# Optimization experiments

Hardware: AMD Instinct MI355X
Metric: run time of the kernel (lower is better)

The kernel has to match this reference:

```python
import jax, jax.numpy as jnp
import numpy as np

N_NODES = 100000
NEG_SLOPE = 0.2


def gat_conv(x, edge_index, W, a_src, a_dst, bias):
    """PyG GATConv, heads=1, concat, add_self_loops=True."""
    N = x.shape[0]
    loop = jnp.arange(N, dtype=edge_index.dtype)
    src = jnp.concatenate([edge_index[0], loop])  # message sources j
    dst = jnp.concatenate([edge_index[1], loop])  # message targets i
    h = x @ W                                      # [N, out]
    asrc = h @ a_src                               # [N]
    adst = h @ a_dst                               # [N]
    e = jax.nn.leaky_relu(asrc[src] + adst[dst], NEG_SLOPE)   # [E+N]
    m = jax.ops.segment_max(e, dst, num_segments=N)           # per-dst max
    w = jnp.exp(e - jax.lax.stop_gradient(m)[dst])
    denom = jax.ops.segment_sum(w, dst, num_segments=N)
    alpha = w / denom[dst]                                     # softmax per dst
    out = jax.ops.segment_sum(alpha[:, None] * h[src], dst, num_segments=N)
    return out + bias


def setup_inputs() -> dict:
    key = jax.random.key(0)
    ks = jax.random.split(key, 16)
    N, E, D = N_NODES, 3200000, 128
    x = jax.random.normal(ks[0], (N, D), dtype=jnp.float32)
    edge_index = jax.random.randint(ks[1], (2, E), 0, N, dtype=jnp.int64)
    def glorot(k, shape):
        fan = sum(shape)
        return jax.random.uniform(k, shape, jnp.float32, -1.0, 1.0) * np.sqrt(6.0 / fan)
    return {
        "x": x,
        "edge_index": edge_index,
        "W1": glorot(ks[2], (D, 16)),
        "a1_src": glorot(ks[3], (16,)),
        "a1_dst": glorot(ks[4], (16,)),
        "b1": jnp.zeros((16,), jnp.float32),
        "W2": glorot(ks[5], (16, 10)),
        "a2_src": glorot(ks[6], (10,)),
        "a2_dst": glorot(ks[7], (10,)),
        "b2": jnp.zeros((10,), jnp.float32),
        "Wl1": glorot(ks[8], (10, 10)),
        "bl1": jnp.zeros((10,), jnp.float32),
        "Wl2": glorot(ks[9], (10, 1)),
        "bl2": jnp.zeros((1,), jnp.float32),
    }


def reference(x, edge_index, W1, a1_src, a1_dst, b1, W2, a2_src, a2_dst, b2,
              Wl1, bl1, Wl2, bl2):
    h = gat_conv(x, edge_index, W1, a1_src, a1_dst, b1)
    h = jax.nn.relu(h)
    h = gat_conv(h, edge_index, W2, a2_src, a2_dst, b2)
    h = h @ Wl1 + bl1
    h = jax.nn.relu(h)
    return h @ Wl2 + bl2  # [N, 1]
```

## Files before the change

### kernel.cpp

```cpp
#include <hip/hip_runtime.h>
#include <hip/hip_fp16.h>


#define NEG 0.2f
#define FSH 7
#define BNODES 128
#define NSBMAX 1024
#define CAP 4608
#define TILE 8192
#define PES 9

__device__ __forceinline__ float lrelu(float x) { return x > 0.0f ? x : NEG * x; }

__device__ __forceinline__ unsigned fenc(float f) {
    unsigned u = __float_as_uint(f);
    return (u & 0x80000000u) ? ~u : (u | 0x80000000u);
}
__device__ __forceinline__ float fdec(unsigned e) {
    return (e & 0x80000000u) ? __uint_as_float(e & 0x7FFFFFFFu) : __uint_as_float(~e);
}

__device__ __forceinline__ float4 ldh4(const __half* h, size_t off) {
    uint2 u = *(const uint2*)(h + off);
    __half2 a = *(__half2*)&u.x, b = *(__half2*)&u.y;
    float2 fa = __half22float2(a), fb = __half22float2(b);
    return make_float4(fa.x, fa.y, fb.x, fb.y);
}

__global__ __launch_bounds__(256) void k_init(unsigned* g, int* chist, int NSB) {
    int i = blockIdx.x * 256 + threadIdx.x;
    if (i < NSB) chist[i] = 0;
    if (i < 2) g[i] = 0u;
}

__global__ __launch_bounds__(256) void k_gemm1(
    const float* __restrict__ x, const float* __restrict__ W1,
    const float* __restrict__ a1s, const float* __restrict__ a1d,
    __half* __restrict__ h1, float* __restrict__ s1, float* __restrict__ d1,
    unsigned* __restrict__ gmax, int N)
{
    __shared__ float sW[128 * 16];
    __shared__ float sx[64 * 132];
    __shared__ float wm[4];
    int tid = threadIdx.x;
    for (int i = tid; i < 2048; i += 256) sW[i] = W1[i];
    int node0 = blockIdx.x * 64;
    for (int i = tid; i < 64 * 32; i += 256) {
        int row = i >> 5, c4 = i & 31;
        int n = node0 + row;
        float4 v = make_float4(0.f, 0.f, 0.f, 0.f);
        if (n < N) v = ((const float4*)x)[(size_t)n * 32 + c4];
        *(float4*)&sx[row * 132 + c4 * 4] = v;
    }
    __syncthreads();

    int node = node0 + (tid >> 2);
    int grp  = tid & 3;
    const float* xr = &sx[(tid >> 2) * 132];
    float4 acc = make_float4(0.f, 0.f, 0.f, 0.f);
#pragma unroll 8
    for (int j = 0; j < 128; ++j) {
        float xv = xr[j];
        float4 w = *(const float4*)&sW[j * 16 + grp * 4];
        acc.x += xv * w.x; acc.y += xv * w.y; acc.z += xv * w.z; acc.w += xv * w.w;
    }
    float4 as = ((const float4*)a1s)[grp];
    float4 ad = ((const float4*)a1d)[grp];
    float sv = acc.x * as.x + acc.y * as.y + acc.z * as.z + acc.w * as.w;
    float dv = acc.x * ad.x + acc.y * ad.y + acc.z * ad.z + acc.w * ad.w;
    sv += __shfl_xor(sv, 1); sv += __shfl_xor(sv, 2);
    dv += __shfl_xor(dv, 1); dv += __shfl_xor(dv, 2);
    if (node < N) {
        __half2 p0 = __floats2half2_rn(acc.x, acc.y);
        __half2 p1 = __floats2half2_rn(acc.z, acc.w);
        uint2 u; u.x = *(unsigned*)&p0; u.y = *(unsigned*)&p1;
        *(uint2*)&h1[(size_t)node * 16 + grp * 4] = u;
        if (grp == 0) { s1[node] = sv; d1[node] = dv; }
    }
    float m = (node < N) ? sv : -3.4e38f;
#pragma unroll
    for (int off = 32; off >= 1; off >>= 1) m = fmaxf(m, __shfl_xor(m, off));
    if ((tid & 63) == 0) wm[tid >> 6] = m;
    __syncthreads();
    if (tid == 0) {
        float b = fmaxf(fmaxf(wm[0], wm[1]), fmaxf(wm[2], wm[3]));
        atomicMax(gmax, fenc(b));
    }
}

__global__ __launch_bounds__(256) void k_chist(const int* __restrict__ edst,
                                               int* __restrict__ chist, int E, int NSB) {
    __shared__ int lc[NSBMAX];
    int tid = threadIdx.x;
    for (int i = tid; i < NSB; i += 256) lc[i] = 0;
    __syncthreads();
    int stride = gridDim.x * 256;
    for (int e = blockIdx.x * 256 + tid; e < E; e += stride)
        atomicAdd(&lc[edst[e] >> FSH], 1);
    __syncthreads();
    for (int i = tid; i < NSB; i += 256) { int v = lc[i]; if (v) atomicAdd(&chist[i], v); }
}

__global__ __launch_bounds__(512) void k_cboffs(const int* __restrict__ chist,
                                                int* __restrict__ cboffs, int* __restrict__ ccur,
                                                int NSB, int E) {
    __shared__ int wsum[8];
    int tid = threadIdx.x;
    int i0 = 2 * tid, i1 = i0 + 1;
    int a = (i0 < NSB) ? chist[i0] : 0;
    int b = (i1 < NSB) ? chist[i1] : 0;
    int s = a + b, pfx = s;
#pragma unroll
    for (int off = 1; off < 64; off <<= 1) {
        int t = __shfl_up(pfx, off, 64);
        if ((tid & 63) >= off) pfx += t;
    }
    if ((tid & 63) == 63) wsum[tid >> 6] = pfx;
    __syncthreads();
    int carry = 0;
    for (int w = 0; w < (tid >> 6); ++w) carry += wsum[w];
    int excl = pfx + carry - s;
    if (i0 < NSB) { cboffs[i0] = excl;     ccur[i0 * 16] = excl; }
    if (i1 < NSB) { cboffs[i1] = excl + a; ccur[i1 * 16] = excl + a; }
    if (tid == 0) cboffs[NSB] = E;
}

__global__ __launch_bounds__(512) void k_csplit(
    const int* __restrict__ esrc, const int* __restrict__ edst,
    int* __restrict__ ccur, unsigned* __restrict__ pairs, int E, int NSB)
{
    __shared__ unsigned lsrt[TILE];
    __shared__ int lhist[NSBMAX];
    __shared__ int lofs[NSBMAX];
    __shared__ int gbase[NSBMAX];
    __shared__ int wsum[8];
    int tid = threadIdx.x;
    int base = blockIdx.x * TILE;
    int tcnt = min(TILE, E - base);
    for (int i = tid; i < NSB; i += 512) lhist[i] = 0;
    __syncthreads();
    for (int i = tid; i < tcnt; i += 512)
        atomicAdd(&lhist[edst[base + i] >> FSH], 1);
    __syncthreads();
    int i0 = 2 * tid, i1 = i0 + 1;
    int a = (i0 < NSB) ? lhist[i0] : 0;
    int b = (i1 < NSB) ? lhist[i1] : 0;
    int s = a + b, pfx = s;
#pragma unroll
    for (int off = 1; off < 64; off <<= 1) {
        int t = __shfl_up(pfx, off, 64);
        if ((tid & 63) >= off) pfx += t;
    }
    if ((tid & 63) == 63) wsum[tid >> 6] = pfx;
    __syncthreads();
    int carry = 0;
    for (int w = 0; w < (tid >> 6); ++w) carry += wsum[w];
    int excl = pfx + carry - s;
    if (i0 < NSB) {
        lofs[i0] = excl;
        gbase[i0] = a ? atomicAdd(&ccur[i0 * 16], a) : 0;
    }
    if (i1 < NSB) {
        lofs[i1] = excl + a;
        gbase[i1] = b ? atomicAdd(&ccur[i1 * 16], b) : 0;
    }
    __syncthreads();
    if (i0 < NSB) lhist[i0] = lofs[i0];
    if (i1 < NSB) lhist[i1] = lofs[i1];
    __syncthreads();
    for (int i = tid; i < tcnt; i += 512) {
        int e = base + i;
        int d = edst[e], srcv = esrc[e];
        int pos = atomicAdd(&lhist[d >> FSH], 1);
        lsrt[pos] = ((unsigned)(d & (BNODES - 1)) << 17) | (unsigned)srcv;
    }
    __syncthreads();
    for (int i = tid; i < tcnt; i += 512) {
        int lo = 0, hi = NSB - 1;
        while (lo < hi) { int mid = (lo + hi + 1) >> 1; if (lofs[mid] <= i) lo = mid; else hi = mid - 1; }
        pairs[gbase[lo] + (i - lofs[lo])] = lsrt[i];
    }
}

__global__ __launch_bounds__(512) void k_agg1(
    const int* __restrict__ boffs, const unsigned* __restrict__ pairs,
    const float* __restrict__ s1, const float* __restrict__ d1, const __half* __restrict__ h1,
    const float* __restrict__ b1, const float* __restrict__ W2,
    const float* __restrict__ a2s, const float* __restrict__ a2d,
    __half* __restrict__ h2, float* __restrict__ s2, float* __restrict__ d2,
    const unsigned* __restrict__ gmax1p, unsigned* __restrict__ gmax2, int N)
{
    __shared__ unsigned srt[CAP];
    __shared__ float accs[BNODES * 17];
    __shared__ int lcnt[BNODES];
    __shared__ int lofs[BNODES + 1];
    __shared__ float dds[BNODES], mbs[BNODES];
    __shared__ float sW[160], sb[16], sas[16], sad[16];
    __shared__ int wsum[8];
    __shared__ float wm[8];

    int tid = threadIdx.x;
    int fb = blockIdx.x;
    if (tid < 160) sW[tid] = W2[tid];
    if (tid < 16) {
        sb[tid]  = b1[tid];
        sas[tid] = (tid < 10) ? a2s[tid] : 0.f;
        sad[tid] = (tid < 10) ? a2d[tid] : 0.f;
    }
    int node0 = fb << FSH;
    float g0 = fdec(*gmax1p);
    if (tid < BNODES) {
        int n = node0 + tid;
        float dd = (n < N) ? d1[n] : 0.f;
        dds[tid] = dd; mbs[tid] = lrelu(g0 + dd);
        lcnt[tid] = 0;
    }
    __syncthreads();

    int jbeg = boffs[fb], jend = boffs[fb + 1];
    int cnt = jend - jbeg;

    unsigned pe[PES];
#pragma unroll
    for (int u = 0; u < PES; ++u) {
        int i = tid + u * 512;
        bool ok = (i < cnt);
        pe[u] = ok ? pairs[jbeg + i] : 0u;
        if (ok) atomicAdd(&lcnt[(pe[u] >> 17) & (BNODES - 1)], 1);
    }
    __syncthreads();
    int c = (tid < BNODES) ? lcnt[tid] : 0;
    int pfx = c;
#pragma unroll
    for (int off = 1; off < 64; off <<= 1) {
        int t = __shfl_up(pfx, off, 64);
        if ((tid & 63) >= off) pfx += t;
    }
    if ((tid & 63) == 63) wsum[tid >> 6] = pfx;
    __syncthreads();
    int carry = 0;
    for (int w = 0; w < (tid >> 6); ++w) carry += wsum[w];
    pfx += carry;
    if (tid < BNODES) { lofs[tid + 1] = pfx; lcnt[tid] = pfx - c; }
    if (tid == 0) lofs[0] = 0;
    __syncthreads();
    int total = lofs[BNODES];

    int gg = tid >> 2, q = tid & 3;
    int n = node0 + gg;
    float4 accv; float den;
    if (n < N) {
        float w = __expf(lrelu(s1[n] + dds[gg]) - mbs[gg]);
        float4 hv = ldh4(h1, (size_t)n * 16 + 4 * q);
        accv = make_float4(w * hv.x, w * hv.y, w * hv.z, w * hv.w);
        den = w;
    } else { accv = make_float4(0.f, 0.f, 0.f, 0.f); den = 0.f; }

    if (total <= CAP && cnt <= CAP) {
#pragma unroll
        for (int u = 0; u < PES; ++u) {
            int i = tid + u * 512;
            if (i < cnt) {
                unsigned p = pe[u];
                int pos = atomicAdd(&lcnt[(p >> 17) & (BNODES - 1)], 1);
                srt[pos] = p & 0x1FFFF;
            }
        }
        __syncthreads();
        {
            float dd = dds[gg], mb = mbs[gg];
            int j = lofs[gg], j1 = lofs[gg + 1];
            for (; j + 4 <= j1; j += 4) {
                int e0 = srt[j], e1 = srt[j + 1], e2 = srt[j + 2], e3 = srt[j + 3];
                float4 H0 = ldh4(h1, (size_t)e0 * 16 + 4 * q);
                float4 H1 = ldh4(h1, (size_t)e1 * 16 + 4 * q);
                float4 H2 = ldh4(h1, (size_t)e2 * 16 + 4 * q);
                float4 H3 = ldh4(h1, (size_t)e3 * 16 + 4 * q);
                int eq = srt[j + q];
                float wq = __expf(lrelu(s1[eq] + dd) - mb);
                float w0 = __shfl(wq, 0, 4), w1 = __shfl(wq, 1, 4);
                float w2 = __shfl(wq, 2, 4), w3 = __shfl(wq, 3, 4);
                accv.x += w0 * H0.x + w1 * H1.x + w2 * H2.x + w3 * H3.x;
                accv.y += w0 * H0.y + w1 * H1.y + w2 * H2.y + w3 * H3.y;
                accv.z += w0 * H0.z + w1 * H1.z + w2 * H2.z + w3 * H3.z;
                accv.w += w0 * H0.w + w1 * H1.w + w2 * H2.w + w3 * H3.w;
                den += (w0 + w1) + (w2 + w3);
            }
            for (; j < j1; ++j) {
                int e0 = srt[j];
                float w0 = __expf(lrelu(s1[e0] + dd) - mb);
                float4 H0 = ldh4(h1, (size_t)e0 * 16 + 4 * q);
                accv.x += w0 * H0.x; accv.y += w0 * H0.y;
                accv.z += w0 * H0.z; accv.w += w0 * H0.w;
                den += w0;
            }
        }
        __syncthreads();
    } else {
        for (int i = tid; i < BNODES * 17; i += 512) accs[i] = 0.f;
        __syncthreads();
        for (int i = tid; i < cnt; i += 512) {
            unsigned p = pairs[jbeg + i];
            int src = p & 0x1FFFF, nl = (p >> 17) & (BNODES - 1);
            float w = __expf(lrelu(s1[src] + dds[nl]) - mbs[nl]);
            float4 H = ldh4(h1, (size_t)src * 16 + 4 * q);
            atomicAdd(&accs[nl * 17 + 4 * q + 0], w * H.x);
            atomicAdd(&accs[nl * 17 + 4 * q + 1], w * H.y);
            atomicAdd(&accs[nl * 17 + 4 * q + 2], w * H.z);
            atomicAdd(&accs[nl * 17 + 4 * q + 3], w * H.w);
            if (q == 0) atomicAdd(&accs[nl * 17 + 16], w);
        }
        __syncthreads();
        accv.x += accs[gg * 17 + 4 * q + 0];
        accv.y += accs[gg * 17 + 4 * q + 1];
        accv.z += accs[gg * 17 + 4 * q + 2];
        accv.w += accs[gg * 17 + 4 * q + 3];
        den += accs[gg * 17 + 16];
        __syncthreads();
    }

    accs[gg * 17 + 4 * q + 0] = accv.x;
    accs[gg * 17 + 4 * q + 1] = accv.y;
    accs[gg * 17 + 4 * q + 2] = accv.z;
    accs[gg * 17 + 4 * q + 3] = accv.w;
    if (q == 0) accs[gg * 17 + 16] = den;
    __syncthreads();

    int g = tid >> 4, k = tid & 15;
    float sval = -3.4e38f;
#pragma unroll
    for (int qq = 0; qq < 4; ++qq) {
        int nl = g * 4 + qq, nn = node0 + nl;
        if (nn >= N) continue;
        float inv = 1.f / accs[nl * 17 + 16];
        float o = fmaxf(accs[nl * 17 + k] * inv + sb[k], 0.f);
        float hh = 0.f;
#pragma unroll
        for (int kk = 0; kk < 16; ++kk) {
            float ov = __shfl(o, kk, 16);
            if (k < 10) hh += ov * sW[kk * 10 + k];
        }
        if (k >= 10) hh = 0.f;
        float ts = hh * sas[k];
        float td = hh * sad[k];
#pragma unroll
        for (int off = 1; off < 16; off <<= 1) {
            ts += __shfl_xor(ts, off, 16);
            td += __shfl_xor(td, off, 16);
        }
        h2[(size_t)nn * 16 + k] = __float2half_rn(hh);
        if (k == 0) { s2[nn] = ts; d2[nn] = td; }
        sval = fmaxf(sval, ts);
    }
    float m = sval;
#pragma unroll
    for (int off = 32; off >= 1; off >>= 1) m = fmaxf(m, __shfl_xor(m, off));
    if ((tid & 63) == 0) wm[tid >> 6] = m;
    __syncthreads();
    if (tid == 0) {
        float bmx = wm[0];
#pragma unroll
        for (int i = 1; i < 8; ++i) bmx = fmaxf(bmx, wm[i]);
        atomicMax(gmax2, fenc(bmx));
    }
}

__global__ __launch_bounds__(512) void k_agg2(
    const int* __restrict__ boffs, const unsigned* __restrict__ pairs,
    const float* __restrict__ s2, const float* __restrict__ d2, const __half* __restrict__ h2,
    const float* __restrict__ b2, const float* __restrict__ Wl1, const float* __restrict__ bl1,
    const float* __restrict__ Wl2, const float* __restrict__ bl2,
    const unsigned* __restrict__ gmax2p, float* __restrict__ out, int N)
{
    __shared__ unsigned srt[CAP];
    __shared__ float accs[BNODES * 17];
    __shared__ int lcnt[BNODES];
    __shared__ int lofs[BNODES + 1];
    __shared__ float dds[BNODES], mbs[BNODES];
    __shared__ float sW1[100], sb1[16], sW2[16], sb2g[16];
    __shared__ float sbl2;
    __shared__ int wsum[8];

    int tid = threadIdx.x;
    int fb = blockIdx.x;
    if (tid < 100) sW1[tid] = Wl1[tid];
    if (tid < 16) {
        sb1[tid]  = (tid < 10) ? bl1[tid] : 0.f;
        sW2[tid]  = (tid < 10) ? Wl2[tid] : 0.f;
        sb2g[tid] = (tid < 10) ? b2[tid]  : 0.f;
    }
    if (tid == 0) sbl2 = bl2[0];
    int node0 = fb << FSH;
    float g0 = fdec(*gmax2p);
    if (tid < BNODES) {
        int n = node0 + tid;
        float dd = (n < N) ? d2[n] : 0.f;
        dds[tid] = dd; mbs[tid] = lrelu(g0 + dd);
        lcnt[tid] = 0;
    }
    __syncthreads();

    int jbeg = boffs[fb], jend = boffs[fb + 1];
    int cnt = jend - jbeg;

    unsigned pe[PES];
#pragma unroll
    for (int u = 0; u < PES; ++u) {
        int i = tid + u * 512;
        bool ok = (i < cnt);
        pe[u] = ok ? pairs[jbeg + i] : 0u;
        if (ok) atomicAdd(&lcnt[(pe[u] >> 17) & (BNODES - 1)], 1);
    }
    __syncthreads();
    int c = (tid < BNODES) ? lcnt[tid] : 0;
    int pfx = c;
#pragma unroll
    for (int off = 1; off < 64; off <<= 1) {
        int t = __shfl_up(pfx, off, 64);
        if ((tid & 63) >= off) pfx += t;
    }
    if ((tid & 63) == 63) wsum[tid >> 6] = pfx;
    __syncthreads();
    int carry = 0;
    for (int w = 0; w < (tid >> 6); ++w) carry += wsum[w];
    pfx += carry;
    if (tid < BNODES) { lofs[tid + 1] = pfx; lcnt[tid] = pfx - c; }
    if (tid == 0) lofs[0] = 0;
    __syncthreads();
    int total = lofs[BNODES];

    int gg = tid >> 2, q = tid & 3;
    int n = node0 + gg;
    float4 accv; float den;
    if (n < N) {
        float w = __expf(lrelu(s2[n] + dds[gg]) - mbs[gg]);
        float4 hv = ldh4(h2, (size_t)n * 16 + 4 * q);
        accv = make_float4(w * hv.x, w * hv.y, w * hv.z, w * hv.w);
        den = w;
    } else { accv = make_float4(0.f, 0.f, 0.f, 0.f); den = 0.f; }

    if (total <= CAP && cnt <= CAP) {
#pragma unroll
        for (int u = 0; u < PES; ++u) {
            int i = tid + u * 512;
            if (i < cnt) {
                unsigned p = pe[u];
                int pos = atomicAdd(&lcnt[(p >> 17) & (BNODES - 1)], 1);
                srt[pos] = p & 0x1FFFF;
            }
        }
        __syncthreads();
        {
            float dd = dds[gg], mb = mbs[gg];
            int j = lofs[gg], j1 = lofs[gg + 1];
            for (; j + 4 <= j1; j += 4) {
                int e0 = srt[j], e1 = srt[j + 1], e2 = srt[j + 2], e3 = srt[j + 3];
                float4 H0 = ldh4(h2, (size_t)e0 * 16 + 4 * q);
                float4 H1 = ldh4(h2, (size_t)e1 * 16 + 4 * q);
                float4 H2 = ldh4(h2, (size_t)e2 * 16 + 4 * q);
                float4 H3 = ldh4(h2, (size_t)e3 * 16 + 4 * q);
                int eq = srt[j + q];
                float wq = __expf(lrelu(s2[eq] + dd) - mb);
                float w0 = __shfl(wq, 0, 4), w1 = __shfl(wq, 1, 4);
                float w2 = __shfl(wq, 2, 4), w3 = __shfl(wq, 3, 4);
                accv.x += w0 * H0.x + w1 * H1.x + w2 * H2.x + w3 * H3.x;
                accv.y += w0 * H0.y + w1 * H1.y + w2 * H2.y + w3 * H3.y;
                accv.z += w0 * H0.z + w1 * H1.z + w2 * H2.z + w3 * H3.z;
                accv.w += w0 * H0.w + w1 * H1.w + w2 * H2.w + w3 * H3.w;
                den += (w0 + w1) + (w2 + w3);
            }
            for (; j < j1; ++j) {
                int e0 = srt[j];
                float w0 = __expf(lrelu(s2[e0] + dd) - mb);
                float4 H0 = ldh4(h2, (size_t)e0 * 16 + 4 * q);
                accv.x += w0 * H0.x; accv.y += w0 * H0.y;
                accv.z += w0 * H0.z; accv.w += w0 * H0.w;
                den += w0;
            }
        }
        __syncthreads();
    } else {
        for (int i = tid; i < BNODES * 17; i += 512) accs[i] = 0.f;
        __syncthreads();
        for (int i = tid; i < cnt; i += 512) {
            unsigned p = pairs[jbeg + i];
            int src = p & 0x1FFFF, nl = (p >> 17) & (BNODES - 1);
            float w = __expf(lrelu(s2[src] + dds[nl]) - mbs[nl]);
            float4 H = ldh4(h2, (size_t)src * 16 + 4 * q);
            atomicAdd(&accs[nl * 17 + 4 * q + 0], w * H.x);
            atomicAdd(&accs[nl * 17 + 4 * q + 1], w * H.y);
            atomicAdd(&accs[nl * 17 + 4 * q + 2], w * H.z);
            atomicAdd(&accs[nl * 17 + 4 * q + 3], w * H.w);
            if (q == 0) atomicAdd(&accs[nl * 17 + 16], w);
        }
        __syncthreads();
        accv.x += accs[gg * 17 + 4 * q + 0];
        accv.y += accs[gg * 17 + 4 * q + 1];
        accv.z += accs[gg * 17 + 4 * q + 2];
        accv.w += accs[gg * 17 + 4 * q + 3];
        den += accs[gg * 17 + 16];
        __syncthreads();
    }

    accs[gg * 17 + 4 * q + 0] = accv.x;
    accs[gg * 17 + 4 * q + 1] = accv.y;
    accs[gg * 17 + 4 * q + 2] = accv.z;
    accs[gg * 17 + 4 * q + 3] = accv.w;
    if (q == 0) accs[gg * 17 + 16] = den;
    __syncthreads();

    int g = tid >> 4, k = tid & 15;
    bool fk = k < 10;
#pragma unroll
    for (int qq = 0; qq < 4; ++qq) {
        int nl = g * 4 + qq, nn = node0 + nl;
        if (nn >= N) continue;
        float inv = 1.f / accs[nl * 17 + 16];
        float o = fk ? accs[nl * 17 + k] * inv + sb2g[k] : 0.f;
        float v = sb1[k];
#pragma unroll
        for (int kk = 0; kk < 10; ++kk) {
            float ov = __shfl(o, kk, 16);
            if (fk) v += ov * sW1[kk * 10 + k];
        }
        float t = fmaxf(v, 0.f);
        float cc = t * sW2[k];
#pragma unroll
        for (int off = 1; off < 16; off <<= 1) cc += __shfl_xor(cc, off, 16);
        if (k == 0) out[nn] = cc + sbl2;
    }
}

extern "C" void kernel_launch(void* const* d_in, const int* in_sizes, int n_in,
                              void* d_out, int out_size, void* d_ws, size_t ws_size,
                              hipStream_t stream)
{
    const float* x   = (const float*)d_in[0];
    const int*   ei  = (const int*)  d_in[1];
    const float* W1  = (const float*)d_in[2];
    const float* a1s = (const float*)d_in[3];
    const float* a1d = (const float*)d_in[4];
    const float* b1  = (const float*)d_in[5];
    const float* W2  = (const float*)d_in[6];
    const float* a2s = (const float*)d_in[7];
    const float* a2d = (const float*)d_in[8];
    const float* b2  = (const float*)d_in[9];
    const float* Wl1 = (const float*)d_in[10];
    const float* bl1 = (const float*)d_in[11];
    const float* Wl2 = (const float*)d_in[12];
    const float* bl2 = (const float*)d_in[13];

    int N = in_sizes[0] / 128;
    int E = in_sizes[1] / 2;
    const int* ei_src = ei;
    const int* ei_dst = ei + E;
    int NSB = (N + BNODES - 1) >> FSH;

    size_t Np = ((size_t)N + 3) & ~(size_t)3;
    size_t need_bytes = (16 + Np * 20) * 4 + ((size_t)NSB * 18 + 1) * 4 + (size_t)E * 4;
    if (ws_size < need_bytes) return;

    float*    ws    = (float*)d_ws;
    unsigned* gmax1 = (unsigned*)d_ws;
    unsigned* gmax2 = gmax1 + 1;
    __half* h1 = (__half*)(ws + 16);
    float* s1 = ws + 16 + Np * 8;
    float* d1 = s1 + Np;
    __half* h2 = (__half*)(d1 + Np);
    float* s2 = (float*)(h2) + Np * 8;
    float* d2 = s2 + Np;
    int* chist  = (int*)(d2 + Np);
    int* cboffs = chist + NSB;
    int* ccur   = cboffs + NSB + 1;
    unsigned* pairs = (unsigned*)(ccur + (size_t)NSB * 16);

    hipLaunchKernelGGL(k_init, dim3((NSB + 255) / 256), dim3(256), 0, stream, gmax1, chist, NSB);
    hipLaunchKernelGGL(k_gemm1, dim3((N + 63) / 64), dim3(256), 0, stream,
                       x, W1, a1s, a1d, h1, s1, d1, gmax1, N);
    hipLaunchKernelGGL(k_chist, dim3(256), dim3(256), 0, stream, ei_dst, chist, E, NSB);
    hipLaunchKernelGGL(k_cboffs, dim3(1), dim3(512), 0, stream, chist, cboffs, ccur, NSB, E);
    hipLaunchKernelGGL(k_csplit, dim3((E + TILE - 1) / TILE), dim3(512), 0, stream,
                       ei_src, ei_dst, ccur, pairs, E, NSB);
    hipLaunchKernelGGL(k_agg1, dim3(NSB), dim3(512), 0, stream,
                       cboffs, pairs, s1, d1, h1, b1, W2, a2s, a2d, h2, s2, d2,
                       gmax1, gmax2, N);
    hipLaunchKernelGGL(k_agg2, dim3(NSB), dim3(512), 0, stream,
                       cboffs, pairs, s2, d2, h2, b2, Wl1, bl1, Wl2, bl2,
                       gmax2, (float*)d_out, N);
}
```

Measured before the change: 292.7 us.

## Replace counting-sort prepass with fixed-capacity per-bucket edge regions

After: 276.3 us, median of 2. -5.6%, faster.

```diff
diff --git a/kernel.cpp b/kernel.cpp
--- a/kernel.cpp
+++ b/kernel.cpp
@@ -6,7 +6,7 @@
 #define FSH 7
 #define BNODES 128
 #define NSBMAX 1024
-#define CAP 4608
+#define CAPB 4608
 #define TILE 8192
 #define PES 9
 
@@ -27,9 +27,9 @@
     return make_float4(fa.x, fa.y, fb.x, fb.y);
 }
 
-__global__ __launch_bounds__(256) void k_init(unsigned* g, int* chist, int NSB) {
+__global__ __launch_bounds__(256) void k_init(unsigned* g, int* bcur, int NSB) {
     int i = blockIdx.x * 256 + threadIdx.x;
-    if (i < NSB) chist[i] = 0;
+    if (i < NSB) bcur[i * 16] = i * CAPB;
     if (i < 2) g[i] = 0u;
 }
 
@@ -88,46 +88,9 @@
     }
 }
 
-__global__ __launch_bounds__(256) void k_chist(const int* __restrict__ edst,
-                                               int* __restrict__ chist, int E, int NSB) {
-    __shared__ int lc[NSBMAX];
-    int tid = threadIdx.x;
-    for (int i = tid; i < NSB; i += 256) lc[i] = 0;
-    __syncthreads();
-    int stride = gridDim.x * 256;
-    for (int e = blockIdx.x * 256 + tid; e < E; e += stride)
-        atomicAdd(&lc[edst[e] >> FSH], 1);
-    __syncthreads();
-    for (int i = tid; i < NSB; i += 256) { int v = lc[i]; if (v) atomicAdd(&chist[i], v); }
-}
-
-__global__ __launch_bounds__(512) void k_cboffs(const int* __restrict__ chist,
-                                                int* __restrict__ cboffs, int* __restrict__ ccur,
-                                                int NSB, int E) {
-    __shared__ int wsum[8];
-    int tid = threadIdx.x;
-    int i0 = 2 * tid, i1 = i0 + 1;
-    int a = (i0 < NSB) ? chist[i0] : 0;
-    int b = (i1 < NSB) ? chist[i1] : 0;
-    int s = a + b, pfx = s;
-#pragma unroll
-    for (int off = 1; off < 64; off <<= 1) {
-        int t = __shfl_up(pfx, off, 64);
-        if ((tid & 63) >= off) pfx += t;
-    }
-    if ((tid & 63) == 63) wsum[tid >> 6] = pfx;
-    __syncthreads();
-    int carry = 0;
-    for (int w = 0; w < (tid >> 6); ++w) carry += wsum[w];
-    int excl = pfx + carry - s;
-    if (i0 < NSB) { cboffs[i0] = excl;     ccur[i0 * 16] = excl; }
-    if (i1 < NSB) { cboffs[i1] = excl + a; ccur[i1 * 16] = excl + a; }
-    if (tid == 0) cboffs[NSB] = E;
-}
-
 __global__ __launch_bounds__(512) void k_csplit(
     const int* __restrict__ esrc, const int* __restrict__ edst,
-    int* __restrict__ ccur, unsigned* __restrict__ pairs, int E, int NSB)
+    int* __restrict__ bcur, unsigned* __restrict__ pairs, int E, int NSB)
 {
     __shared__ unsigned lsrt[TILE];
     __shared__ int lhist[NSBMAX];
@@ -158,11 +121,11 @@
     int excl = pfx + carry - s;
     if (i0 < NSB) {
         lofs[i0] = excl;
-        gbase[i0] = a ? atomicAdd(&ccur[i0 * 16], a) : 0;
+        gbase[i0] = a ? atomicAdd(&bcur[i0 * 16], a) : 0;
     }
     if (i1 < NSB) {
         lofs[i1] = excl + a;
-        gbase[i1] = b ? atomicAdd(&ccur[i1 * 16], b) : 0;
+        gbase[i1] = b ? atomicAdd(&bcur[i1 * 16], b) : 0;
     }
     __syncthreads();
     if (i0 < NSB) lhist[i0] = lofs[i0];
@@ -178,19 +141,21 @@
     for (int i = tid; i < tcnt; i += 512) {
         int lo = 0, hi = NSB - 1;
         while (lo < hi) { int mid = (lo + hi + 1) >> 1; if (lofs[mid] <= i) lo = mid; else hi = mid - 1; }
-        pairs[gbase[lo] + (i - lofs[lo])] = lsrt[i];
+        int gp = gbase[lo] + (i - lofs[lo]);
+        if (gp < (lo + 1) * CAPB) pairs[gp] = lsrt[i];
     }
 }
 
 __global__ __launch_bounds__(512) void k_agg1(
-    const int* __restrict__ boffs, const unsigned* __restrict__ pairs,
+    const int* __restrict__ bcur, const unsigned* __restrict__ pairs,
+    const int* __restrict__ esrc, const int* __restrict__ edst,
     const float* __restrict__ s1, const float* __restrict__ d1, const __half* __restrict__ h1,
     const float* __restrict__ b1, const float* __restrict__ W2,
     const float* __restrict__ a2s, const float* __restrict__ a2d,
     __half* __restrict__ h2, float* __restrict__ s2, float* __restrict__ d2,
-    const unsigned* __restrict__ gmax1p, unsigned* __restrict__ gmax2, int N)
+    const unsigned* __restrict__ gmax1p, unsigned* __restrict__ gmax2, int N, int E)
 {
-    __shared__ unsigned srt[CAP];
+    __shared__ unsigned srt[CAPB];
     __shared__ float accs[BNODES * 17];
     __shared__ int lcnt[BNODES];
     __shared__ int lofs[BNODES + 1];
@@ -217,46 +182,35 @@
     }
     __syncthreads();
 
-    int jbeg = boffs[fb], jend = boffs[fb + 1];
-    int cnt = jend - jbeg;
-
-    unsigned pe[PES];
-#pragma unroll
-    for (int u = 0; u < PES; ++u) {
-        int i = tid + u * 512;
-        bool ok = (i < cnt);
-        pe[u] = ok ? pairs[jbeg + i] : 0u;
-        if (ok) atomicAdd(&lcnt[(pe[u] >> 17) & (BNODES - 1)], 1);
-    }
-    __syncthreads();
-    int c = (tid < BNODES) ? lcnt[tid] : 0;
-    int pfx = c;
-#pragma unroll
-    for (int off = 1; off < 64; off <<= 1) {
-        int t = __shfl_up(pfx, off, 64);
-        if ((tid & 63) >= off) pfx += t;
-    }
-    if ((tid & 63) == 63) wsum[tid >> 6] = pfx;
-    __syncthreads();
-    int carry = 0;
-    for (int w = 0; w < (tid >> 6); ++w) carry += wsum[w];
-    pfx += carry;
-    if (tid < BNODES) { lofs[tid + 1] = pfx; lcnt[tid] = pfx - c; }
-    if (tid == 0) lofs[0] = 0;
-    __syncthreads();
-    int total = lofs[BNODES];
-
+    int rbase = fb * CAPB;
+    int cnt = bcur[fb * 16] - rbase;
     int gg = tid >> 2, q = tid & 3;
-    int n = node0 + gg;
-    float4 accv; float den;
-    if (n < N) {
-        float w = __expf(lrelu(s1[n] + dds[gg]) - mbs[gg]);
-        float4 hv = ldh4(h1, (size_t)n * 16 + 4 * q);
-        accv = make_float4(w * hv.x, w * hv.y, w * hv.z, w * hv.w);
-        den = w;
-    } else { accv = make_float4(0.f, 0.f, 0.f, 0.f); den = 0.f; }
-
-    if (total <= CAP && cnt <= CAP) {
+
+    if (cnt <= CAPB) {
+        unsigned pe[PES];
+#pragma unroll
+        for (int u = 0; u < PES; ++u) {
+            int i = tid + u * 512;
+            bool ok = (i < cnt);
+            pe[u] = ok ? pairs[rbase + i] : 0u;
+            if (ok) atomicAdd(&lcnt[(pe[u] >> 17) & (BNODES - 1)], 1);
+        }
+        __syncthreads();
+        int c = (tid < BNODES) ? lcnt[tid] : 0;
+        int pfx = c;
+#pragma unroll
+        for (int off = 1; off < 64; off <<= 1) {
+            int t = __shfl_up(pfx, off, 64);
+            if ((tid & 63) >= off) pfx += t;
+        }
+        if ((tid & 63) == 63) wsum[tid >> 6] = pfx;
+        __syncthreads();
+        int carry = 0;
+        for (int w = 0; w < (tid >> 6); ++w) carry += wsum[w];
+        pfx += carry;
+        if (tid < BNODES) { lofs[tid + 1] = pfx; lcnt[tid] = pfx - c; }
+        if (tid == 0) lofs[0] = 0;
+        __syncthreads();
 #pragma unroll
         for (int u = 0; u < PES; ++u) {
             int i = tid + u * 512;
@@ -267,6 +221,15 @@
             }
         }
         __syncthreads();
+
+        int n = node0 + gg;
+        float4 accv; float den;
+        if (n < N) {
+            float w = __expf(lrelu(s1[n] + dds[gg]) - mbs[gg]);
+            float4 hv = ldh4(h1, (size_t)n * 16 + 4 * q);
+            accv = make_float4(w * hv.x, w * hv.y, w * hv.z, w * hv.w);
+            den = w;
+        } else { accv = make_float4(0.f, 0.f, 0.f, 0.f); den = 0.f; }
         {
             float dd = dds[gg], mb = mbs[gg];
             int j = lofs[gg], j1 = lofs[gg + 1];
@@ -295,36 +258,38 @@
                 den += w0;
             }
         }
+        accs[gg * 17 + 4 * q + 0] = accv.x;
+        accs[gg * 17 + 4 * q + 1] = accv.y;
+        accs[gg * 17 + 4 * q + 2] = accv.z;
+        accs[gg * 17 + 4 * q + 3] = accv.w;
+        if (q == 0) accs[gg * 17 + 16] = den;
         __syncthreads();
     } else {
         for (int i = tid; i < BNODES * 17; i += 512) accs[i] = 0.f;
         __syncthreads();
-        for (int i = tid; i < cnt; i += 512) {
-            unsigned p = pairs[jbeg + i];
-            int src = p & 0x1FFFF, nl = (p >> 17) & (BNODES - 1);
+        if (tid < BNODES) {
+            int n = node0 + tid;
+            if (n < N) {
+                float w = __expf(lrelu(s1[n] + dds[tid]) - mbs[tid]);
+#pragma unroll
+                for (int t = 0; t < 16; ++t)
+                    accs[tid * 17 + t] = w * __half2float(h1[(size_t)n * 16 + t]);
+                accs[tid * 17 + 16] = w;
+            }
+        }
+        __syncthreads();
+        for (int i = tid; i < E; i += 512) {
+            int d = edst[i];
+            if ((d >> FSH) != fb) continue;
+            int nl = d & (BNODES - 1), src = esrc[i];
             float w = __expf(lrelu(s1[src] + dds[nl]) - mbs[nl]);
-            float4 H = ldh4(h1, (size_t)src * 16 + 4 * q);
-            atomicAdd(&accs[nl * 17 + 4 * q + 0], w * H.x);
-            atomicAdd(&accs[nl * 17 + 4 * q + 1], w * H.y);
-            atomicAdd(&accs[nl * 17 + 4 * q + 2], w * H.z);
-            atomicAdd(&accs[nl * 17 + 4 * q + 3], w * H.w);
-            if (q == 0) atomicAdd(&accs[nl * 17 + 16], w);
-        }
-        __syncthreads();
-        accv.x += accs[gg * 17 + 4 * q + 0];
-        accv.y += accs[gg * 17 + 4 * q + 1];
-        accv.z += accs[gg * 17 + 4 * q + 2];
-        accv.w += accs[gg * 17 + 4 * q + 3];
-        den += accs[gg * 17 + 16];
-        __syncthreads();
-    }
-
-    accs[gg * 17 + 4 * q + 0] = accv.x;
-    accs[gg * 17 + 4 * q + 1] = accv.y;
-    accs[gg * 17 + 4 * q + 2] = accv.z;
-    accs[gg * 17 + 4 * q + 3] = accv.w;
-    if (q == 0) accs[gg * 17 + 16] = den;
-    __syncthreads();
+#pragma unroll
+            for (int t = 0; t < 16; ++t)
+                atomicAdd(&accs[nl * 17 + t], w * __half2float(h1[(size_t)src * 16 + t]));
+            atomicAdd(&accs[nl * 17 + 16], w);
+        }
+        __syncthreads();
+    }
 
     int g = tid >> 4, k = tid & 15;
     float sval = -3.4e38f;
@@ -366,13 +331,14 @@
 }
 
 __global__ __launch_bounds__(512) void k_agg2(
-    const int* __restrict__ boffs, const unsigned* __restrict__ pairs,
+    const int* __restrict__ bcur, const unsigned* __restrict__ pairs,
+    const int* __restrict__ esrc, const int* __restrict__ edst,
     const float* __restrict__ s2, const float* __restrict__ d2, const __half* __restrict__ h2,
     const float* __restrict__ b2, const float* __restrict__ Wl1, const float* __restrict__ bl1,
     const float* __restrict__ Wl2, const float* __restrict__ bl2,
-    const unsigned* __restrict__ gmax2p, float* __restrict__ out, int N)
+    const unsigned* __restrict__ gmax2p, float* __restrict__ out, int N, int E)
 {
-    __shared__ unsigned srt[CAP];
+    __shared__ unsigned srt[CAPB];
     __shared__ float accs[BNODES * 17];
     __shared__ int lcnt[BNODES];
     __shared__ int lofs[BNODES + 1];
@@ -400,46 +366,35 @@
     }
     __syncthreads();
 
-    int jbeg = boffs[fb], jend = boffs[fb + 1];
-    int cnt = jend - jbeg;
-
-    unsigned pe[PES];
-#pragma unroll
-    for (int u = 0; u < PES; ++u) {
-        int i = tid + u * 512;
-        bool ok = (i < cnt);
-        pe[u] = ok ? pairs[jbeg + i] : 0u;
-        if (ok) atomicAdd(&lcnt[(pe[u] >> 17) & (BNODES - 1)], 1);
-    }
-    __syncthreads();
-    int c = (tid < BNODES) ? lcnt[tid] : 0;
-    int pfx = c;
-#pragma unroll
-    for (int off = 1; off < 64; off <<= 1) {
-        int t = __shfl_up(pfx, off, 64);
-        if ((tid & 63) >= off) pfx += t;
-    }
-    if ((tid & 63) == 63) wsum[tid >> 6] = pfx;
-    __syncthreads();
-    int carry = 0;
-    for (int w = 0; w < (tid >> 6); ++w) carry += wsum[w];
-    pfx += carry;
-    if (tid < BNODES) { lofs[tid + 1] = pfx; lcnt[tid] = pfx - c; }
-    if (tid == 0) lofs[0] = 0;
-    __syncthreads();
-    int total = lofs[BNODES];
-
+    int rbase = fb * CAPB;
+    int cnt = bcur[fb * 16] - rbase;
     int gg = tid >> 2, q = tid & 3;
-    int n = node0 + gg;
-    float4 accv; float den;
-    if (n < N) {
-        float w = __expf(lrelu(s2[n] + dds[gg]) - mbs[gg]);
-        float4 hv = ldh4(h2, (size_t)n * 16 + 4 * q);
-        accv = make_float4(w * hv.x, w * hv.y, w * hv.z, w * hv.w);
-        den = w;
-    } else { accv = make_float4(0.f, 0.f, 0.f, 0.f); den = 0.f; }
-
-    if (total <= CAP && cnt <= CAP) {
+
+    if (cnt <= CAPB) {
+        unsigned pe[PES];
+#pragma unroll
+        for (int u = 0; u < PES; ++u) {
+            int i = tid + u * 512;
+            bool ok = (i < cnt);
+            pe[u] = ok ? pairs[rbase + i] : 0u;
+            if (ok) atomicAdd(&lcnt[(pe[u] >> 17) & (BNODES - 1)], 1);
+        }
+        __syncthreads();
+        int c = (tid < BNODES) ? lcnt[tid] : 0;
+        int pfx = c;
+#pragma unroll
+        for (int off = 1; off < 64; off <<= 1) {
+            int t = __shfl_up(pfx, off, 64);
+            if ((tid & 63) >= off) pfx += t;
+        }
+        if ((tid & 63) == 63) wsum[tid >> 6] = pfx;
+        __syncthreads();
+        int carry = 0;
+        for (int w = 0; w < (tid >> 6); ++w) carry += wsum[w];
+        pfx += carry;
+        if (tid < BNODES) { lofs[tid + 1] = pfx; lcnt[tid] = pfx - c; }
+        if (tid == 0) lofs[0] = 0;
+        __syncthreads();
 #pragma unroll
         for (int u = 0; u < PES; ++u) {
             int i = tid + u * 512;
@@ -450,6 +405,15 @@
             }
         }
         __syncthreads();
+
+        int n = node0 + gg;
+        float4 accv; float den;
+        if (n < N) {
+            float w = __expf(lrelu(s2[n] + dds[gg]) - mbs[gg]);
+            float4 hv = ldh4(h2, (size_t)n * 16 + 4 * q);
+            accv = make_float4(w * hv.x, w * hv.y, w * hv.z, w * hv.w);
+            den = w;
+        } else { accv = make_float4(0.f, 0.f, 0.f, 0.f); den = 0.f; }
         {
             float dd = dds[gg], mb = mbs[gg];
             int j = lofs[gg], j1 = lofs[gg + 1];
@@ -478,36 +442,38 @@
                 den += w0;
             }
         }
+        accs[gg * 17 + 4 * q + 0] = accv.x;
+        accs[gg * 17 + 4 * q + 1] = accv.y;
+        accs[gg * 17 + 4 * q + 2] = accv.z;
+        accs[gg * 17 + 4 * q + 3] = accv.w;
+        if (q == 0) accs[gg * 17 + 16] = den;
         __syncthreads();
     } else {
         for (int i = tid; i < BNODES * 17; i += 512) accs[i] = 0.f;
         __syncthreads();
-        for (int i = tid; i < cnt; i += 512) {
-            unsigned p = pairs[jbeg + i];
-            int src = p & 0x1FFFF, nl = (p >> 17) & (BNODES - 1);
+        if (tid < BNODES) {
+            int n = node0 + tid;
+            if (n < N) {
+                float w = __expf(lrelu(s2[n] + dds[tid]) - mbs[tid]);
+#pragma unroll
+                for (int t = 0; t < 16; ++t)
+                    accs[tid * 17 + t] = w * __half2float(h2[(size_t)n * 16 + t]);
+                accs[tid * 17 + 16] = w;
+            }
+        }
+        __syncthreads();
+        for (int i = tid; i < E; i += 512) {
+            int d = edst[i];
+            if ((d >> FSH) != fb) continue;
+            int nl = d & (BNODES - 1), src = esrc[i];
             float w = __expf(lrelu(s2[src] + dds[nl]) - mbs[nl]);
-            float4 H = ldh4(h2, (size_t)src * 16 + 4 * q);
-            atomicAdd(&accs[nl * 17 + 4 * q + 0], w * H.x);
-            atomicAdd(&accs[nl * 17 + 4 * q + 1], w * H.y);
-            atomicAdd(&accs[nl * 17 + 4 * q + 2], w * H.z);
-            atomicAdd(&accs[nl * 17 + 4 * q + 3], w * H.w);
-            if (q == 0) atomicAdd(&accs[nl * 17 + 16], w);
-        }
-        __syncthreads();
-        accv.x += accs[gg * 17 + 4 * q + 0];
-        accv.y += accs[gg * 17 + 4 * q + 1];
-        accv.z += accs[gg * 17 + 4 * q + 2];
-        accv.w += accs[gg * 17 + 4 * q + 3];
-        den += accs[gg * 17 + 16];
-        __syncthreads();
-    }
-
-    accs[gg * 17 + 4 * q + 0] = accv.x;
-    accs[gg * 17 + 4 * q + 1] = accv.y;
-    accs[gg * 17 + 4 * q + 2] = accv.z;
-    accs[gg * 17 + 4 * q + 3] = accv.w;
-    if (q == 0) accs[gg * 17 + 16] = den;
-    __syncthreads();
+#pragma unroll
+            for (int t = 0; t < 16; ++t)
+                atomicAdd(&accs[nl * 17 + t], w * __half2float(h2[(size_t)src * 16 + t]));
+            atomicAdd(&accs[nl * 17 + 16], w);
+        }
+        __syncthreads();
+    }
 
     int g = tid >> 4, k = tid & 15;
     bool fk = k < 10;
@@ -557,7 +523,7 @@
     int NSB = (N + BNODES - 1) >> FSH;
 
     size_t Np = ((size_t)N + 3) & ~(size_t)3;
-    size_t need_bytes = (16 + Np * 20) * 4 + ((size_t)NSB * 18 + 1) * 4 + (size_t)E * 4;
+    size_t need_bytes = (16 + Np * 20) * 4 + (size_t)NSB * 16 * 4 + (size_t)NSB * CAPB * 4;
     if (ws_size < need_bytes) return;
 
     float*    ws    = (float*)d_ws;
@@ -569,22 +535,18 @@
     __half* h2 = (__half*)(d1 + Np);
     float* s2 = (float*)(h2) + Np * 8;
     float* d2 = s2 + Np;
-    int* chist  = (int*)(d2 + Np);
-    int* cboffs = chist + NSB;
-    int* ccur   = cboffs + NSB + 1;
-    unsigned* pairs = (unsigned*)(ccur + (size_t)NSB * 16);
-
-    hipLaunchKernelGGL(k_init, dim3((NSB + 255) / 256), dim3(256), 0, stream, gmax1, chist, NSB);
+    int* bcur = (int*)(d2 + Np);
+    unsigned* pairs = (unsigned*)(bcur + (size_t)NSB * 16);
+
+    hipLaunchKernelGGL(k_init, dim3((NSB + 255) / 256), dim3(256), 0, stream, gmax1, bcur, NSB);
     hipLaunchKernelGGL(k_gemm1, dim3((N + 63) / 64), dim3(256), 0, stream,
                        x, W1, a1s, a1d, h1, s1, d1, gmax1, N);
-    hipLaunchKernelGGL(k_chist, dim3(256), dim3(256), 0, stream, ei_dst, chist, E, NSB);
-    hipLaunchKernelGGL(k_cboffs, dim3(1), dim3(512), 0, stream, chist, cboffs, ccur, NSB, E);
     hipLaunchKernelGGL(k_csplit, dim3((E + TILE - 1) / TILE), dim3(512), 0, stream,
-                       ei_src, ei_dst, ccur, pairs, E, NSB);
+                       ei_src, ei_dst, bcur, pairs, E, NSB);
     hipLaunchKernelGGL(k_agg1, dim3(NSB), dim3(512), 0, stream,
-                       cboffs, pairs, s1, d1, h1, b1, W2, a2s, a2d, h2, s2, d2,
-                       gmax1, gmax2, N);
+                       bcur, pairs, ei_src, ei_dst, s1, d1, h1, b1, W2, a2s, a2d,
+                       h2, s2, d2, gmax1, gmax2, N, E);
     hipLaunchKernelGGL(k_agg2, dim3(NSB), dim3(512), 0, stream,
-                       cboffs, pairs, s2, d2, h2, b2, Wl1, bl1, Wl2, bl2,
-                       gmax2, (float*)d_out, N);
-}
+                       bcur, pairs, ei_src, ei_dst, s2, d2, h2, b2, Wl1, bl1, Wl2, bl2,
+                       gmax2, (float*)d_out, N, E);
+}
```
